# Kernel optimization log

Hardware: AMD Instinct MI355X
Metric: run time of the kernel (lower is better)

The kernel has to match this reference:

```python
import jax, jax.numpy as jnp
import numpy as np

B, N, G, E = 4, 8192, 512, 512
D = 3 * E  # fused channel dim = 1536
BN_EPS = 1e-5


def setup_inputs() -> dict:
    key = jax.random.key(0)
    ks = jax.random.split(key, 8)
    f32 = jnp.float32
    return {
        "xyz": jax.random.normal(ks[0], (B, N, 3), f32),
        "centers": jax.random.normal(ks[1], (B, G, 3), f32),
        "H4": jax.random.normal(ks[2], (B, G, E), f32),
        "H8": jax.random.normal(ks[3], (B, G, E), f32),
        "H12": jax.random.normal(ks[4], (B, G, E), f32),
        "w1": jax.random.normal(ks[5], (512, D), f32) * 0.02,
        "b1": jnp.zeros((512,), f32),
        "g1": jnp.ones((512,), f32),
        "be1": jnp.zeros((512,), f32),
        "m1": jnp.zeros((512,), f32),
        "v1": jnp.ones((512,), f32),
        "w2": jax.random.normal(ks[6], (512, 512), f32) * 0.02,
        "b2": jnp.zeros((512,), f32),
        "g2": jnp.ones((512,), f32),
        "be2": jnp.zeros((512,), f32),
        "m2": jnp.zeros((512,), f32),
        "v2": jnp.ones((512,), f32),
    }


def _bn(x, gamma, beta, mean, var):
    # BatchNorm1d, eval mode with running stats (per-channel, last axis)
    return (x - mean) * jax.lax.rsqrt(var + BN_EPS) * gamma + beta


def reference(xyz, centers, H4, H8, H12,
              w1, b1, g1, be1, m1, v1,
              w2, b2, g2, be2, m2, v2):
    fused = jnp.concatenate([H4, H8, H12], axis=-1)  # [B,G,D]
    # squared pairwise distances [B,N,G]
    d = (jnp.sum(xyz * xyz, axis=-1, keepdims=True)
         + jnp.sum(centers * centers, axis=-1)[:, None, :]
         - 2.0 * jnp.einsum('bnc,bgc->bng', xyz, centers))
    neg_d3, idx = jax.lax.top_k(-d, 3)  # 3 smallest distances, ascending
    d3 = -neg_d3  # [B,N,3]
    recip = 1.0 / (d3 + 1e-8)
    w = recip / jnp.sum(recip, axis=-1, keepdims=True)  # [B,N,3]
    # gather neighbor features: [B,N,3,D]
    gathered = jax.vmap(lambda f, i: f[i])(fused, idx)
    interp = jnp.einsum('bnk,bnkd->bnd', w, gathered)  # [B,N,D]
    # 1x1 conv == per-point linear; conv -> BN(eval) -> ReLU, twice
    h = jax.nn.relu(_bn(interp @ w1.T + b1, g1, be1, m1, v1))
    h = jax.nn.relu(_bn(h @ w2.T + b2, g2, be2, m2, v2))
    return h  # [B,N,512]
```

## Files before the change

### kernel.cpp

```cpp
#include <hip/hip_runtime.h>
#include <stdint.h>

#define NB 4
#define NP 8192
#define NG 512
#define DF 1536
#define NC 512

using f32x4   = __attribute__((ext_vector_type(4))) float;
using bf16x8  = __attribute__((ext_vector_type(8))) __bf16;
using ushort8v = __attribute__((ext_vector_type(8))) unsigned short;


__device__ __forceinline__ unsigned short f32_to_bf16(float f) {
  unsigned int u = __float_as_uint(f);
  u += 0x7fffu + ((u >> 16) & 1u);
  return (unsigned short)(u >> 16);
}

__global__ __launch_bounds__(256) void setup_kernel(
    const float* __restrict__ xyz, const float* __restrict__ centers,
    const float* __restrict__ H4, const float* __restrict__ H8,
    const float* __restrict__ H12,
    const float* __restrict__ w1, const float* __restrict__ w2,
    const float* __restrict__ g1, const float* __restrict__ be1,
    const float* __restrict__ m1, const float* __restrict__ v1,
    const float* __restrict__ g2, const float* __restrict__ be2,
    const float* __restrict__ m2, const float* __restrict__ v2,
    unsigned short* __restrict__ fswz, unsigned short* __restrict__ w1s,
    unsigned short* __restrict__ w2s,
    int* __restrict__ oidx, float* __restrict__ ow,
    float* __restrict__ s1, float* __restrict__ t1,
    float* __restrict__ s2, float* __restrict__ t2)
{
  __shared__ float4 cs[4 * 129];
  const int bx = blockIdx.x, tid = threadIdx.x;

  if (bx < 512) {
    const int b = bx >> 7;
    for (int i = tid; i < NG; i += 256) {
      float c0 = centers[((size_t)b * NG + i) * 3 + 0];
      float c1 = centers[((size_t)b * NG + i) * 3 + 1];
      float c2 = centers[((size_t)b * NG + i) * 3 + 2];
      float4 v; v.x = c0; v.y = c1; v.z = c2; v.w = c0 * c0 + c1 * c1 + c2 * c2;
      cs[(i >> 7) * 129 + (i & 127)] = v;
    }
    __syncthreads();
    const int t = (bx & 127) * 256 + tid;
    const int p = t >> 2, q = t & 3;
    const size_t pi = (size_t)b * NP + p;
    const float x0 = xyz[pi * 3 + 0], x1 = xyz[pi * 3 + 1], x2 = xyz[pi * 3 + 2];
    const float xx = x0 * x0 + x1 * x1 + x2 * x2;
    float d0 = 3.4e38f, d1 = 3.4e38f, d2 = 3.4e38f;
    int i0 = 0, i1 = 0, i2 = 0;
    const int gbase = q * 128;
    const float4* csq = cs + q * 129;
#pragma unroll 4
    for (int j = 0; j < 128; ++j) {
      float4 c = csq[j];
      float d = xx + c.w - 2.0f * (x0 * c.x + x1 * c.y + x2 * c.z);
      int g = gbase + j;
      bool c0 = d < d0, c1 = d < d1, c2 = d < d2;
      float nd2 = c1 ? d1 : (c2 ? d : d2); int ni2 = c1 ? i1 : (c2 ? g : i2);
      float nd1 = c0 ? d0 : (c1 ? d : d1); int ni1 = c0 ? i0 : (c1 ? g : i1);
      d0 = c0 ? d : d0;                    i0 = c0 ? g : i0;
      d1 = nd1; i1 = ni1; d2 = nd2; i2 = ni2;
    }
#pragma unroll
    for (int off = 1; off <= 2; off <<= 1) {
      float e0 = __shfl_xor(d0, off), e1 = __shfl_xor(d1, off), e2 = __shfl_xor(d2, off);
      int j0 = __shfl_xor(i0, off), j1 = __shfl_xor(i1, off), j2 = __shfl_xor(i2, off);
#pragma unroll
      for (int s = 0; s < 3; ++s) {
        float e = (s == 0) ? e0 : (s == 1 ? e1 : e2);
        int   j = (s == 0) ? j0 : (s == 1 ? j1 : j2);
        bool c0 = (e < d0) || (e == d0 && j < i0);
        bool c1 = (e < d1) || (e == d1 && j < i1);
        bool c2 = (e < d2) || (e == d2 && j < i2);
        float nd2 = c1 ? d1 : (c2 ? e : d2); int ni2 = c1 ? i1 : (c2 ? j : i2);
        float nd1 = c0 ? d0 : (c1 ? e : d1); int ni1 = c0 ? i0 : (c1 ? j : i1);
        d0 = c0 ? e : d0;                    i0 = c0 ? j : i0;
        d1 = nd1; i1 = ni1; d2 = nd2; i2 = ni2;
      }
    }
    if (q == 0) {
      float r0 = 1.0f / (d0 + 1e-8f), r1 = 1.0f / (d1 + 1e-8f), r2 = 1.0f / (d2 + 1e-8f);
      float inv = 1.0f / (r0 + r1 + r2);
      ow[pi * 3 + 0] = r0 * inv; ow[pi * 3 + 1] = r1 * inv; ow[pi * 3 + 2] = r2 * inv;
      oidx[pi * 3 + 0] = i0; oidx[pi * 3 + 1] = i1; oidx[pi * 3 + 2] = i2;
    }
  } else if (bx < 2048) {
    const int qd = (bx - 512) * 256 + tid;
    const int L = qd & 63, t2 = qd >> 6;
    const int kc = t2 % 48, mg = t2 / 48;
    const int m = mg * 16 + (L & 15);
    const int k = kc * 32 + (L >> 4) * 8;
    const float* src = (k < 512) ? H4 : (k < 1024 ? H8 : H12);
    const float* sp = &src[(size_t)m * 512 + (k & 511)];
    float4 va = *(const float4*)sp, vb = *(const float4*)(sp + 4);
    ushort8v o;
    o[0] = f32_to_bf16(va.x); o[1] = f32_to_bf16(va.y);
    o[2] = f32_to_bf16(va.z); o[3] = f32_to_bf16(va.w);
    o[4] = f32_to_bf16(vb.x); o[5] = f32_to_bf16(vb.y);
    o[6] = f32_to_bf16(vb.z); o[7] = f32_to_bf16(vb.w);
    *(ushort8v*)&fswz[((size_t)(mg * 48 + kc)) * 512 + L * 8] = o;
  } else if (bx < 2432) {
    const int qd = (bx - 2048) * 256 + tid;
    const int L = qd & 63, t2 = qd >> 6;
    const int kc = t2 % 48, ng = t2 / 48;
    const int n = ng * 16 + (L & 15);
    const int k = kc * 32 + (L >> 4) * 8;
    const float* sp = &w1[(size_t)n * 1536 + k];
    float4 va = *(const float4*)sp, vb = *(const float4*)(sp + 4);
    ushort8v o;
    o[0] = f32_to_bf16(va.x); o[1] = f32_to_bf16(va.y);
    o[2] = f32_to_bf16(va.z); o[3] = f32_to_bf16(va.w);
    o[4] = f32_to_bf16(vb.x); o[5] = f32_to_bf16(vb.y);
    o[6] = f32_to_bf16(vb.z); o[7] = f32_to_bf16(vb.w);
    *(ushort8v*)&w1s[((size_t)(ng * 48 + kc)) * 512 + L * 8] = o;
  } else if (bx < 2560) {
    const int qd = (bx - 2432) * 256 + tid;
    const int L = qd & 63, t2 = qd >> 6;
    const int kc = t2 & 15, ng = t2 >> 4;
    const int n = ng * 16 + (L & 15);
    const int k = kc * 32 + (L >> 4) * 8;
    const float* sp = &w2[(size_t)n * 512 + k];
    float4 va = *(const float4*)sp, vb = *(const float4*)(sp + 4);
    ushort8v o;
    o[0] = f32_to_bf16(va.x); o[1] = f32_to_bf16(va.y);
    o[2] = f32_to_bf16(va.z); o[3] = f32_to_bf16(va.w);
    o[4] = f32_to_bf16(vb.x); o[5] = f32_to_bf16(vb.y);
    o[6] = f32_to_bf16(vb.z); o[7] = f32_to_bf16(vb.w);
    *(ushort8v*)&w2s[((size_t)(ng * 16 + kc)) * 512 + L * 8] = o;
  } else {
    for (int i = tid; i < 512; i += 256) {
      float sa = g1[i] / sqrtf(v1[i] + 1e-5f);
      s1[i] = sa; t1[i] = be1[i] - m1[i] * sa;
      float sb = g2[i] / sqrtf(v2[i] + 1e-5f);
      s2[i] = sb; t2[i] = be2[i] - m2[i] * sb;
    }
  }
}

__global__ __launch_bounds__(256) void gemm1_kernel(
    const unsigned short* __restrict__ Aswz, const unsigned short* __restrict__ Bswz,
    float* __restrict__ Amat,
    const float* __restrict__ svec, const float* __restrict__ bvec,
    const float* __restrict__ tvec)
{
  __shared__ float red[64 * 65];
  const int tid = threadIdx.x, lane = tid & 63, wv = tid >> 6;
  const int m0 = (blockIdx.x >> 3) * 64;
  const int n0 = (blockIdx.x & 7) * 64;

  const unsigned short* Ap = Aswz + ((size_t)((m0 >> 4)) * 48 + wv * 12) * 512 + lane * 8;
  const unsigned short* Bp = Bswz + ((size_t)((n0 >> 4)) * 48 + wv * 12) * 512 + lane * 8;

  f32x4 acc[4][4];
#pragma unroll
  for (int i = 0; i < 4; ++i)
#pragma unroll
    for (int j = 0; j < 4; ++j) acc[i][j] = (f32x4){0.f, 0.f, 0.f, 0.f};

  bf16x8 af[4], bfr[4], afn[4], bfn[4];
#pragma unroll
  for (int i = 0; i < 4; ++i) {
    af[i]  = __builtin_bit_cast(bf16x8, *(const ushort8v*)(Ap + (size_t)i * 48 * 512));
    bfr[i] = __builtin_bit_cast(bf16x8, *(const ushort8v*)(Bp + (size_t)i * 48 * 512));
  }
#pragma unroll 1
  for (int kc = 0; kc < 12; ++kc) {
    if (kc < 11) {
#pragma unroll
      for (int i = 0; i < 4; ++i) {
        afn[i] = __builtin_bit_cast(bf16x8, *(const ushort8v*)(Ap + (size_t)i * 48 * 512 + (kc + 1) * 512));
        bfn[i] = __builtin_bit_cast(bf16x8, *(const ushort8v*)(Bp + (size_t)i * 48 * 512 + (kc + 1) * 512));
      }
    }
#pragma unroll
    for (int mi = 0; mi < 4; ++mi)
#pragma unroll
      for (int ni = 0; ni < 4; ++ni)
        acc[mi][ni] = __builtin_amdgcn_mfma_f32_16x16x32_bf16(af[mi], bfr[ni], acc[mi][ni], 0, 0, 0);
#pragma unroll
    for (int i = 0; i < 4; ++i) { af[i] = afn[i]; bfr[i] = bfn[i]; }
  }

  for (int w = 0; w < 4; ++w) {
    if (wv == w) {
#pragma unroll
      for (int mi = 0; mi < 4; ++mi)
#pragma unroll
        for (int ni = 0; ni < 4; ++ni) {
          int col = ni * 16 + (lane & 15);
#pragma unroll
          for (int r = 0; r < 4; ++r) {
            int row = mi * 16 + (lane >> 4) * 4 + r;
            if (w == 0) red[row * 65 + col] = acc[mi][ni][r];
            else        red[row * 65 + col] += acc[mi][ni][r];
          }
        }
    }
    __syncthreads();
  }
#pragma unroll
  for (int i = 0; i < 4; ++i) {
    int row = (tid >> 4) + i * 16;
    int col = (tid & 15) * 4;
    float4 v = *(const float4*)&red[row * 65 + col];
    int n = n0 + col;
    v.x = svec[n + 0] * (v.x + bvec[n + 0]) + tvec[n + 0];
    v.y = svec[n + 1] * (v.y + bvec[n + 1]) + tvec[n + 1];
    v.z = svec[n + 2] * (v.z + bvec[n + 2]) + tvec[n + 2];
    v.w = svec[n + 3] * (v.w + bvec[n + 3]) + tvec[n + 3];
    *(float4*)&Amat[(size_t)(m0 + row) * 512 + n] = v;
  }
}

__global__ __launch_bounds__(256) void interp_kernel(
    const float* __restrict__ Amat, const int* __restrict__ nidx,
    const float* __restrict__ nw, unsigned short* __restrict__ h1s)
{
  const int lane = threadIdx.x & 63, wv = threadIdx.x >> 6;
  const int pg = blockIdx.x * 4 + wv;
  const int p = pg * 16 + (lane & 15);
  const int b = p >> 13;
  const int i0 = nidx[p * 3 + 0], i1 = nidx[p * 3 + 1], i2 = nidx[p * 3 + 2];
  const float w0 = nw[p * 3 + 0], w1v = nw[p * 3 + 1], w2v = nw[p * 3 + 2];
  const float* A0 = Amat + ((size_t)(b * 512 + i0)) * 512;
  const float* A1 = Amat + ((size_t)(b * 512 + i1)) * 512;
  const float* A2 = Amat + ((size_t)(b * 512 + i2)) * 512;
  const int cbase = (lane >> 4) * 8;
  unsigned short* wp = h1s + ((size_t)pg * 16) * 512 + lane * 8;
#pragma unroll 4
  for (int cc = 0; cc < 16; ++cc) {
    const int c = cc * 32 + cbase;
    float4 a0a = *(const float4*)&A0[c], a0b = *(const float4*)&A0[c + 4];
    float4 a1a = *(const float4*)&A1[c], a1b = *(const float4*)&A1[c + 4];
    float4 a2a = *(const float4*)&A2[c], a2b = *(const float4*)&A2[c + 4];
    ushort8v o;
    o[0] = f32_to_bf16(fmaxf(w0 * a0a.x + w1v * a1a.x + w2v * a2a.x, 0.f));
    o[1] = f32_to_bf16(fmaxf(w0 * a0a.y + w1v * a1a.y + w2v * a2a.y, 0.f));
    o[2] = f32_to_bf16(fmaxf(w0 * a0a.z + w1v * a1a.z + w2v * a2a.z, 0.f));
    o[3] = f32_to_bf16(fmaxf(w0 * a0a.w + w1v * a1a.w + w2v * a2a.w, 0.f));
    o[4] = f32_to_bf16(fmaxf(w0 * a0b.x + w1v * a1b.x + w2v * a2b.x, 0.f));
    o[5] = f32_to_bf16(fmaxf(w0 * a0b.y + w1v * a1b.y + w2v * a2b.y, 0.f));
    o[6] = f32_to_bf16(fmaxf(w0 * a0b.z + w1v * a1b.z + w2v * a2b.z, 0.f));
    o[7] = f32_to_bf16(fmaxf(w0 * a0b.w + w1v * a1b.w + w2v * a2b.w, 0.f));
    *(ushort8v*)(wp + (size_t)cc * 512) = o;
  }
}

__global__ __launch_bounds__(256) void gemm2_kernel(
    const unsigned short* __restrict__ Aswz, const unsigned short* __restrict__ Bswz,
    float* __restrict__ outp,
    const float* __restrict__ svec, const float* __restrict__ bvec,
    const float* __restrict__ tvec)
{
  const int tid = threadIdx.x, lane = tid & 63, wv = tid >> 6;
  const int wm = wv >> 1, wn = wv & 1;
  const int L = blockIdx.x;
  const int xcd = L & 7, slot = L >> 3;
  const int mloc = slot >> 2, nt = slot & 3;
  const int m0 = (xcd * 32 + mloc) * 128, n0 = nt * 128;

  const unsigned short* Ap = Aswz + ((size_t)((m0 >> 4) + wm * 4) * 16) * 512 + lane * 8;
  const unsigned short* Bp = Bswz + ((size_t)((n0 >> 4) + wn * 4) * 16) * 512 + lane * 8;

  f32x4 acc[4][4];
#pragma unroll
  for (int i = 0; i < 4; ++i)
#pragma unroll
    for (int j = 0; j < 4; ++j) acc[i][j] = (f32x4){0.f, 0.f, 0.f, 0.f};

  bf16x8 af[4], bfr[4], afn[4], bfn[4];
#pragma unroll
  for (int i = 0; i < 4; ++i) {
    af[i]  = __builtin_bit_cast(bf16x8, *(const ushort8v*)(Ap + (size_t)i * 16 * 512));
    bfr[i] = __builtin_bit_cast(bf16x8, *(const ushort8v*)(Bp + (size_t)i * 16 * 512));
  }
#pragma unroll 1
  for (int kc = 0; kc < 16; ++kc) {
    if (kc < 15) {
#pragma unroll
      for (int i = 0; i < 4; ++i) {
        afn[i] = __builtin_bit_cast(bf16x8, *(const ushort8v*)(Ap + (size_t)i * 16 * 512 + (kc + 1) * 512));
        bfn[i] = __builtin_bit_cast(bf16x8, *(const ushort8v*)(Bp + (size_t)i * 16 * 512 + (kc + 1) * 512));
      }
    }
#pragma unroll
    for (int mi = 0; mi < 4; ++mi)
#pragma unroll
      for (int ni = 0; ni < 4; ++ni)
        acc[mi][ni] = __builtin_amdgcn_mfma_f32_16x16x32_bf16(af[mi], bfr[ni], acc[mi][ni], 0, 0, 0);
#pragma unroll
    for (int i = 0; i < 4; ++i) { af[i] = afn[i]; bfr[i] = bfn[i]; }
  }

#pragma unroll
  for (int mi = 0; mi < 4; ++mi) {
    int mbase = m0 + wm * 64 + mi * 16 + (lane >> 4) * 4;
#pragma unroll
    for (int ni = 0; ni < 4; ++ni) {
      int n = n0 + wn * 64 + ni * 16 + (lane & 15);
      float s = svec[n], bb = bvec[n], t = tvec[n];
      f32x4 v = acc[mi][ni];
#pragma unroll
      for (int r = 0; r < 4; ++r) {
        float val = fmaxf(s * (v[r] + bb) + t, 0.f);
        outp[(size_t)(mbase + r) * 512 + n] = val;
      }
    }
  }
}

extern "C" void kernel_launch(void* const* d_in, const int* in_sizes, int n_in,
                              void* d_out, int out_size, void* d_ws, size_t ws_size,
                              hipStream_t stream) {
  const float* xyz     = (const float*)d_in[0];
  const float* centers = (const float*)d_in[1];
  const float* H4      = (const float*)d_in[2];
  const float* H8      = (const float*)d_in[3];
  const float* H12     = (const float*)d_in[4];
  const float* w1      = (const float*)d_in[5];
  const float* b1      = (const float*)d_in[6];
  const float* g1      = (const float*)d_in[7];
  const float* be1     = (const float*)d_in[8];
  const float* m1      = (const float*)d_in[9];
  const float* v1      = (const float*)d_in[10];
  const float* w2      = (const float*)d_in[11];
  const float* b2      = (const float*)d_in[12];
  const float* g2      = (const float*)d_in[13];
  const float* be2     = (const float*)d_in[14];
  const float* m2      = (const float*)d_in[15];
  const float* v2      = (const float*)d_in[16];
  float* outp = (float*)d_out;

  char* ws = (char*)d_ws;
  unsigned short* fswz = (unsigned short*)(ws);
  unsigned short* w1s  = (unsigned short*)(ws + 6291456);
  unsigned short* w2s  = (unsigned short*)(ws + 7864320);
  float*          Amat = (float*)         (ws + 8388608);
  unsigned short* h1s  = (unsigned short*)(ws + 12582912);
  int*            nidx = (int*)           (ws + 46137344);
  float*          nw   = (float*)         (ws + 46530560);
  float*          s1   = (float*)         (ws + 46923776);
  float* t1 = s1 + 512; float* s2 = t1 + 512; float* t2 = s2 + 512;

  setup_kernel<<<2561, 256, 0, stream>>>(
      xyz, centers, H4, H8, H12, w1, w2,
      g1, be1, m1, v1, g2, be2, m2, v2,
      fswz, w1s, w2s, nidx, nw, s1, t1, s2, t2);
  gemm1_kernel<<<256, 256, 0, stream>>>(fswz, w1s, Amat, s1, b1, t1);
  interp_kernel<<<512, 256, 0, stream>>>(Amat, nidx, nw, h1s);
  gemm2_kernel<<<1024, 256, 0, stream>>>(h1s, w2s, outp, s2, b2, t2);
}
```

Baseline: 188.4 us.

## Fuse all stages into one cooperative persistent kernel with grid syncs and bf16 intermediate

Merges setup, gemm1, interpolation and gemm2 into a single cooperative kernel of 512 blocks that loops over work units and separates phases with grid-wide syncs, removing the gaps between kernel launches. The gemm1 output is now stored as bf16 instead of fp32, which halves the traffic for the gather-heavy interpolation. gemm1 tiles shrink to 32 rows so its work spreads over 512 blocks. A fallback path launches the four phases as separate kernels if cooperative launch fails. The costs are grid-sync overhead, a launch-bound occupancy limit, and an extra bf16 rounding before interpolation.

```diff
diff --git a/kernel.cpp b/kernel.cpp
--- a/kernel.cpp
+++ b/kernel.cpp
@@ -1,14 +1,15 @@
 #include <hip/hip_runtime.h>
+#include <hip/hip_cooperative_groups.h>
 #include <stdint.h>
 
-#define NB 4
 #define NP 8192
 #define NG 512
 #define DF 1536
-#define NC 512
-
-using f32x4   = __attribute__((ext_vector_type(4))) float;
-using bf16x8  = __attribute__((ext_vector_type(8))) __bf16;
+
+namespace cg = cooperative_groups;
+
+using f32x4    = __attribute__((ext_vector_type(4))) float;
+using bf16x8   = __attribute__((ext_vector_type(8))) __bf16;
 using ushort8v = __attribute__((ext_vector_type(8))) unsigned short;
 
 
@@ -17,39 +18,35 @@
   u += 0x7fffu + ((u >> 16) & 1u);
   return (unsigned short)(u >> 16);
 }
-
-__global__ __launch_bounds__(256) void setup_kernel(
-    const float* __restrict__ xyz, const float* __restrict__ centers,
-    const float* __restrict__ H4, const float* __restrict__ H8,
-    const float* __restrict__ H12,
-    const float* __restrict__ w1, const float* __restrict__ w2,
-    const float* __restrict__ g1, const float* __restrict__ be1,
-    const float* __restrict__ m1, const float* __restrict__ v1,
-    const float* __restrict__ g2, const float* __restrict__ be2,
-    const float* __restrict__ m2, const float* __restrict__ v2,
-    unsigned short* __restrict__ fswz, unsigned short* __restrict__ w1s,
-    unsigned short* __restrict__ w2s,
-    int* __restrict__ oidx, float* __restrict__ ow,
-    float* __restrict__ s1, float* __restrict__ t1,
-    float* __restrict__ s2, float* __restrict__ t2)
-{
-  __shared__ float4 cs[4 * 129];
-  const int bx = blockIdx.x, tid = threadIdx.x;
-
-  if (bx < 512) {
-    const int b = bx >> 7;
+__device__ __forceinline__ float bf2f(unsigned short u) {
+  return __uint_as_float(((unsigned)u) << 16);
+}
+
+struct FusedArgs {
+  const float *xyz, *centers, *H4, *H8, *H12, *w1, *w2;
+  const float *g1, *be1, *m1, *v1, *g2, *be2, *m2, *v2, *b1, *b2;
+  unsigned short *fswz, *w1s, *w2s, *Amatb, *h1s;
+  int *nidx; float *nw, *s1, *t1, *s2, *t2;
+  float *outp;
+};
+
+__device__ void phase_setup(const FusedArgs& a, char* smem, int w) {
+  const int tid = threadIdx.x;
+  if (w < 512) {
+    float4* cs = (float4*)smem;
+    const int b = w >> 7;
     for (int i = tid; i < NG; i += 256) {
-      float c0 = centers[((size_t)b * NG + i) * 3 + 0];
-      float c1 = centers[((size_t)b * NG + i) * 3 + 1];
-      float c2 = centers[((size_t)b * NG + i) * 3 + 2];
+      float c0 = a.centers[((size_t)b * NG + i) * 3 + 0];
+      float c1 = a.centers[((size_t)b * NG + i) * 3 + 1];
+      float c2 = a.centers[((size_t)b * NG + i) * 3 + 2];
       float4 v; v.x = c0; v.y = c1; v.z = c2; v.w = c0 * c0 + c1 * c1 + c2 * c2;
       cs[(i >> 7) * 129 + (i & 127)] = v;
     }
     __syncthreads();
-    const int t = (bx & 127) * 256 + tid;
+    const int t = (w & 127) * 256 + tid;
     const int p = t >> 2, q = t & 3;
     const size_t pi = (size_t)b * NP + p;
-    const float x0 = xyz[pi * 3 + 0], x1 = xyz[pi * 3 + 1], x2 = xyz[pi * 3 + 2];
+    const float x0 = a.xyz[pi * 3 + 0], x1 = a.xyz[pi * 3 + 1], x2 = a.xyz[pi * 3 + 2];
     const float xx = x0 * x0 + x1 * x1 + x2 * x2;
     float d0 = 3.4e38f, d1 = 3.4e38f, d2 = 3.4e38f;
     int i0 = 0, i1 = 0, i2 = 0;
@@ -86,16 +83,17 @@
     if (q == 0) {
       float r0 = 1.0f / (d0 + 1e-8f), r1 = 1.0f / (d1 + 1e-8f), r2 = 1.0f / (d2 + 1e-8f);
       float inv = 1.0f / (r0 + r1 + r2);
-      ow[pi * 3 + 0] = r0 * inv; ow[pi * 3 + 1] = r1 * inv; ow[pi * 3 + 2] = r2 * inv;
-      oidx[pi * 3 + 0] = i0; oidx[pi * 3 + 1] = i1; oidx[pi * 3 + 2] = i2;
-    }
-  } else if (bx < 2048) {
-    const int qd = (bx - 512) * 256 + tid;
+      a.nw[pi * 3 + 0] = r0 * inv; a.nw[pi * 3 + 1] = r1 * inv; a.nw[pi * 3 + 2] = r2 * inv;
+      a.nidx[pi * 3 + 0] = i0; a.nidx[pi * 3 + 1] = i1; a.nidx[pi * 3 + 2] = i2;
+    }
+    __syncthreads();
+  } else if (w < 2048) {
+    const int qd = (w - 512) * 256 + tid;
     const int L = qd & 63, t2 = qd >> 6;
     const int kc = t2 % 48, mg = t2 / 48;
     const int m = mg * 16 + (L & 15);
     const int k = kc * 32 + (L >> 4) * 8;
-    const float* src = (k < 512) ? H4 : (k < 1024 ? H8 : H12);
+    const float* src = (k < 512) ? a.H4 : (k < 1024 ? a.H8 : a.H12);
     const float* sp = &src[(size_t)m * 512 + (k & 511)];
     float4 va = *(const float4*)sp, vb = *(const float4*)(sp + 4);
     ushort8v o;
@@ -103,93 +101,92 @@
     o[2] = f32_to_bf16(va.z); o[3] = f32_to_bf16(va.w);
     o[4] = f32_to_bf16(vb.x); o[5] = f32_to_bf16(vb.y);
     o[6] = f32_to_bf16(vb.z); o[7] = f32_to_bf16(vb.w);
-    *(ushort8v*)&fswz[((size_t)(mg * 48 + kc)) * 512 + L * 8] = o;
-  } else if (bx < 2432) {
-    const int qd = (bx - 2048) * 256 + tid;
+    *(ushort8v*)&a.fswz[((size_t)(mg * 48 + kc)) * 512 + L * 8] = o;
+  } else if (w < 2432) {
+    const int qd = (w - 2048) * 256 + tid;
     const int L = qd & 63, t2 = qd >> 6;
     const int kc = t2 % 48, ng = t2 / 48;
     const int n = ng * 16 + (L & 15);
     const int k = kc * 32 + (L >> 4) * 8;
-    const float* sp = &w1[(size_t)n * 1536 + k];
+    const float* sp = &a.w1[(size_t)n * 1536 + k];
     float4 va = *(const float4*)sp, vb = *(const float4*)(sp + 4);
     ushort8v o;
     o[0] = f32_to_bf16(va.x); o[1] = f32_to_bf16(va.y);
     o[2] = f32_to_bf16(va.z); o[3] = f32_to_bf16(va.w);
     o[4] = f32_to_bf16(vb.x); o[5] = f32_to_bf16(vb.y);
     o[6] = f32_to_bf16(vb.z); o[7] = f32_to_bf16(vb.w);
-    *(ushort8v*)&w1s[((size_t)(ng * 48 + kc)) * 512 + L * 8] = o;
-  } else if (bx < 2560) {
-    const int qd = (bx - 2432) * 256 + tid;
+    *(ushort8v*)&a.w1s[((size_t)(ng * 48 + kc)) * 512 + L * 8] = o;
+  } else if (w < 2560) {
+    const int qd = (w - 2432) * 256 + tid;
     const int L = qd & 63, t2 = qd >> 6;
     const int kc = t2 & 15, ng = t2 >> 4;
     const int n = ng * 16 + (L & 15);
     const int k = kc * 32 + (L >> 4) * 8;
-    const float* sp = &w2[(size_t)n * 512 + k];
+    const float* sp = &a.w2[(size_t)n * 512 + k];
     float4 va = *(const float4*)sp, vb = *(const float4*)(sp + 4);
     ushort8v o;
     o[0] = f32_to_bf16(va.x); o[1] = f32_to_bf16(va.y);
     o[2] = f32_to_bf16(va.z); o[3] = f32_to_bf16(va.w);
     o[4] = f32_to_bf16(vb.x); o[5] = f32_to_bf16(vb.y);
     o[6] = f32_to_bf16(vb.z); o[7] = f32_to_bf16(vb.w);
-    *(ushort8v*)&w2s[((size_t)(ng * 16 + kc)) * 512 + L * 8] = o;
+    *(ushort8v*)&a.w2s[((size_t)(ng * 16 + kc)) * 512 + L * 8] = o;
   } else {
     for (int i = tid; i < 512; i += 256) {
-      float sa = g1[i] / sqrtf(v1[i] + 1e-5f);
-      s1[i] = sa; t1[i] = be1[i] - m1[i] * sa;
-      float sb = g2[i] / sqrtf(v2[i] + 1e-5f);
-      s2[i] = sb; t2[i] = be2[i] - m2[i] * sb;
-    }
-  }
-}
-
-__global__ __launch_bounds__(256) void gemm1_kernel(
-    const unsigned short* __restrict__ Aswz, const unsigned short* __restrict__ Bswz,
-    float* __restrict__ Amat,
-    const float* __restrict__ svec, const float* __restrict__ bvec,
-    const float* __restrict__ tvec)
-{
-  __shared__ float red[64 * 65];
+      float sa = a.g1[i] / sqrtf(a.v1[i] + 1e-5f);
+      a.s1[i] = sa; a.t1[i] = a.be1[i] - a.m1[i] * sa;
+      float sb = a.g2[i] / sqrtf(a.v2[i] + 1e-5f);
+      a.s2[i] = sb; a.t2[i] = a.be2[i] - a.m2[i] * sb;
+    }
+  }
+}
+
+__device__ void phase_gemm1(const FusedArgs& a, char* smem) {
+  float* red = (float*)smem;
   const int tid = threadIdx.x, lane = tid & 63, wv = tid >> 6;
-  const int m0 = (blockIdx.x >> 3) * 64;
-  const int n0 = (blockIdx.x & 7) * 64;
-
-  const unsigned short* Ap = Aswz + ((size_t)((m0 >> 4)) * 48 + wv * 12) * 512 + lane * 8;
-  const unsigned short* Bp = Bswz + ((size_t)((n0 >> 4)) * 48 + wv * 12) * 512 + lane * 8;
-
-  f32x4 acc[4][4];
+  const int blk = blockIdx.x;
+  const int m0 = (blk >> 3) * 32;
+  const int n0 = (blk & 7) * 64;
+  const unsigned short* Ap = a.fswz + ((size_t)(m0 >> 4) * 48 + wv * 12) * 512 + lane * 8;
+  const unsigned short* Bp = a.w1s  + ((size_t)(n0 >> 4) * 48 + wv * 12) * 512 + lane * 8;
+
+  f32x4 acc[2][4];
+#pragma unroll
+  for (int i = 0; i < 2; ++i)
+#pragma unroll
+    for (int j = 0; j < 4; ++j) acc[i][j] = (f32x4){0.f, 0.f, 0.f, 0.f};
+
+  bf16x8 af[2], bfr[4], afn[2], bfn[4];
+#pragma unroll
+  for (int i = 0; i < 2; ++i)
+    af[i]  = __builtin_bit_cast(bf16x8, *(const ushort8v*)(Ap + (size_t)i * 48 * 512));
 #pragma unroll
   for (int i = 0; i < 4; ++i)
-#pragma unroll
-    for (int j = 0; j < 4; ++j) acc[i][j] = (f32x4){0.f, 0.f, 0.f, 0.f};
-
-  bf16x8 af[4], bfr[4], afn[4], bfn[4];
-#pragma unroll
-  for (int i = 0; i < 4; ++i) {
-    af[i]  = __builtin_bit_cast(bf16x8, *(const ushort8v*)(Ap + (size_t)i * 48 * 512));
     bfr[i] = __builtin_bit_cast(bf16x8, *(const ushort8v*)(Bp + (size_t)i * 48 * 512));
-  }
 #pragma unroll 1
   for (int kc = 0; kc < 12; ++kc) {
     if (kc < 11) {
 #pragma unroll
-      for (int i = 0; i < 4; ++i) {
+      for (int i = 0; i < 2; ++i)
         afn[i] = __builtin_bit_cast(bf16x8, *(const ushort8v*)(Ap + (size_t)i * 48 * 512 + (kc + 1) * 512));
+#pragma unroll
+      for (int i = 0; i < 4; ++i)
         bfn[i] = __builtin_bit_cast(bf16x8, *(const ushort8v*)(Bp + (size_t)i * 48 * 512 + (kc + 1) * 512));
-      }
-    }
-#pragma unroll
-    for (int mi = 0; mi < 4; ++mi)
+    }
+#pragma unroll
+    for (int mi = 0; mi < 2; ++mi)
 #pragma unroll
       for (int ni = 0; ni < 4; ++ni)
         acc[mi][ni] = __builtin_amdgcn_mfma_f32_16x16x32_bf16(af[mi], bfr[ni], acc[mi][ni], 0, 0, 0);
 #pragma unroll
-    for (int i = 0; i < 4; ++i) { af[i] = afn[i]; bfr[i] = bfn[i]; }
+    for (int i = 0; i < 2; ++i) af[i] = afn[i];
+#pragma unroll
+    for (int i = 0; i < 4; ++i) bfr[i] = bfn[i];
   }
 
   for (int w = 0; w < 4; ++w) {
     if (wv == w) {
 #pragma unroll
-      for (int mi = 0; mi < 4; ++mi)
+      for (int mi = 0; mi < 2; ++mi)
 #pragma unroll
         for (int ni = 0; ni < 4; ++ni) {
           int col = ni * 16 + (lane & 15);
@@ -203,69 +200,55 @@
     }
     __syncthreads();
   }
-#pragma unroll
-  for (int i = 0; i < 4; ++i) {
-    int row = (tid >> 4) + i * 16;
-    int col = (tid & 15) * 4;
-    float4 v = *(const float4*)&red[row * 65 + col];
-    int n = n0 + col;
-    v.x = svec[n + 0] * (v.x + bvec[n + 0]) + tvec[n + 0];
-    v.y = svec[n + 1] * (v.y + bvec[n + 1]) + tvec[n + 1];
-    v.z = svec[n + 2] * (v.z + bvec[n + 2]) + tvec[n + 2];
-    v.w = svec[n + 3] * (v.w + bvec[n + 3]) + tvec[n + 3];
-    *(float4*)&Amat[(size_t)(m0 + row) * 512 + n] = v;
-  }
-}
-
-__global__ __launch_bounds__(256) void interp_kernel(
-    const float* __restrict__ Amat, const int* __restrict__ nidx,
-    const float* __restrict__ nw, unsigned short* __restrict__ h1s)
-{
-  const int lane = threadIdx.x & 63, wv = threadIdx.x >> 6;
+  const int row = tid >> 3;
+  const int col = (tid & 7) * 8;
+  ushort8v o;
+#pragma unroll
+  for (int j = 0; j < 8; ++j) {
+    int n = n0 + col + j;
+    float v = red[row * 65 + col + j];
+    o[j] = f32_to_bf16(a.s1[n] * (v + a.b1[n]) + a.t1[n]);
+  }
+  *(ushort8v*)&a.Amatb[(size_t)(m0 + row) * 512 + n0 + col] = o;
+}
+
+__device__ void phase_interp(const FusedArgs& a) {
+  const int tid = threadIdx.x, lane = tid & 63, wv = tid >> 6;
   const int pg = blockIdx.x * 4 + wv;
   const int p = pg * 16 + (lane & 15);
   const int b = p >> 13;
-  const int i0 = nidx[p * 3 + 0], i1 = nidx[p * 3 + 1], i2 = nidx[p * 3 + 2];
-  const float w0 = nw[p * 3 + 0], w1v = nw[p * 3 + 1], w2v = nw[p * 3 + 2];
-  const float* A0 = Amat + ((size_t)(b * 512 + i0)) * 512;
-  const float* A1 = Amat + ((size_t)(b * 512 + i1)) * 512;
-  const float* A2 = Amat + ((size_t)(b * 512 + i2)) * 512;
+  const int i0 = a.nidx[p * 3 + 0], i1 = a.nidx[p * 3 + 1], i2 = a.nidx[p * 3 + 2];
+  const float w0 = a.nw[p * 3 + 0], w1v = a.nw[p * 3 + 1], w2v = a.nw[p * 3 + 2];
+  const unsigned short* A0 = a.Amatb + ((size_t)(b * 512 + i0)) * 512;
+  const unsigned short* A1 = a.Amatb + ((size_t)(b * 512 + i1)) * 512;
+  const unsigned short* A2 = a.Amatb + ((size_t)(b * 512 + i2)) * 512;
   const int cbase = (lane >> 4) * 8;
-  unsigned short* wp = h1s + ((size_t)pg * 16) * 512 + lane * 8;
+  unsigned short* wp = a.h1s + ((size_t)pg * 16) * 512 + lane * 8;
 #pragma unroll 4
   for (int cc = 0; cc < 16; ++cc) {
     const int c = cc * 32 + cbase;
-    float4 a0a = *(const float4*)&A0[c], a0b = *(const float4*)&A0[c + 4];
-    float4 a1a = *(const float4*)&A1[c], a1b = *(const float4*)&A1[c + 4];
-    float4 a2a = *(const float4*)&A2[c], a2b = *(const float4*)&A2[c + 4];
+    ushort8v u0 = *(const ushort8v*)&A0[c];
+    ushort8v u1 = *(const ushort8v*)&A1[c];
+    ushort8v u2 = *(const ushort8v*)&A2[c];
     ushort8v o;
-    o[0] = f32_to_bf16(fmaxf(w0 * a0a.x + w1v * a1a.x + w2v * a2a.x, 0.f));
-    o[1] = f32_to_bf16(fmaxf(w0 * a0a.y + w1v * a1a.y + w2v * a2a.y, 0.f));
-    o[2] = f32_to_bf16(fmaxf(w0 * a0a.z + w1v * a1a.z + w2v * a2a.z, 0.f));
-    o[3] = f32_to_bf16(fmaxf(w0 * a0a.w + w1v * a1a.w + w2v * a2a.w, 0.f));
-    o[4] = f32_to_bf16(fmaxf(w0 * a0b.x + w1v * a1b.x + w2v * a2b.x, 0.f));
-    o[5] = f32_to_bf16(fmaxf(w0 * a0b.y + w1v * a1b.y + w2v * a2b.y, 0.f));
-    o[6] = f32_to_bf16(fmaxf(w0 * a0b.z + w1v * a1b.z + w2v * a2b.z, 0.f));
-    o[7] = f32_to_bf16(fmaxf(w0 * a0b.w + w1v * a1b.w + w2v * a2b.w, 0.f));
+#pragma unroll
+    for (int j = 0; j < 8; ++j) {
+      float v = w0 * bf2f(u0[j]) + w1v * bf2f(u1[j]) + w2v * bf2f(u2[j]);
+      o[j] = f32_to_bf16(fmaxf(v, 0.f));
+    }
     *(ushort8v*)(wp + (size_t)cc * 512) = o;
   }
 }
 
-__global__ __launch_bounds__(256) void gemm2_kernel(
-    const unsigned short* __restrict__ Aswz, const unsigned short* __restrict__ Bswz,
-    float* __restrict__ outp,
-    const float* __restrict__ svec, const float* __restrict__ bvec,
-    const float* __restrict__ tvec)
-{
+__device__ void phase_gemm2(const FusedArgs& a, int L) {
   const int tid = threadIdx.x, lane = tid & 63, wv = tid >> 6;
   const int wm = wv >> 1, wn = wv & 1;
-  const int L = blockIdx.x;
   const int xcd = L & 7, slot = L >> 3;
   const int mloc = slot >> 2, nt = slot & 3;
   const int m0 = (xcd * 32 + mloc) * 128, n0 = nt * 128;
 
-  const unsigned short* Ap = Aswz + ((size_t)((m0 >> 4) + wm * 4) * 16) * 512 + lane * 8;
-  const unsigned short* Bp = Bswz + ((size_t)((n0 >> 4) + wn * 4) * 16) * 512 + lane * 8;
+  const unsigned short* Ap = a.h1s + ((size_t)((m0 >> 4) + wm * 4) * 16) * 512 + lane * 8;
+  const unsigned short* Bp = a.w2s + ((size_t)((n0 >> 4) + wn * 4) * 16) * 512 + lane * 8;
 
   f32x4 acc[4][4];
 #pragma unroll
@@ -303,55 +286,92 @@
 #pragma unroll
     for (int ni = 0; ni < 4; ++ni) {
       int n = n0 + wn * 64 + ni * 16 + (lane & 15);
-      float s = svec[n], bb = bvec[n], t = tvec[n];
+      float s = a.s2[n], bb = a.b2[n], t = a.t2[n];
       f32x4 v = acc[mi][ni];
 #pragma unroll
       for (int r = 0; r < 4; ++r) {
         float val = fmaxf(s * (v[r] + bb) + t, 0.f);
-        outp[(size_t)(mbase + r) * 512 + n] = val;
+        a.outp[(size_t)(mbase + r) * 512 + n] = val;
       }
     }
   }
+}
+
+__global__ __launch_bounds__(256, 2) void fused_kernel(FusedArgs a) {
+  __shared__ __align__(16) char smem[8448];
+  cg::grid_group grid = cg::this_grid();
+  const int blk = blockIdx.x;
+  for (int u = blk; u <= 2560; u += 512) phase_setup(a, smem, u);
+  grid.sync();
+  phase_gemm1(a, smem);
+  grid.sync();
+  phase_interp(a);
+  grid.sync();
+  phase_gemm2(a, blk);
+  phase_gemm2(a, blk + 512);
+}
+
+__global__ __launch_bounds__(256) void k_setup(FusedArgs a) {
+  __shared__ __align__(16) char smem[8448];
+  for (int u = blockIdx.x; u <= 2560; u += 512) phase_setup(a, smem, u);
+}
+__global__ __launch_bounds__(256) void k_gemm1(FusedArgs a) {
+  __shared__ __align__(16) char smem[8448];
+  phase_gemm1(a, smem);
+}
+__global__ __launch_bounds__(256) void k_interp(FusedArgs a) { phase_interp(a); }
+__global__ __launch_bounds__(256) void k_gemm2(FusedArgs a) {
+  phase_gemm2(a, blockIdx.x);
+  phase_gemm2(a, blockIdx.x + 512);
 }
 
 extern "C" void kernel_launch(void* const* d_in, const int* in_sizes, int n_in,
                               void* d_out, int out_size, void* d_ws, size_t ws_size,
                               hipStream_t stream) {
-  const float* xyz     = (const float*)d_in[0];
-  const float* centers = (const float*)d_in[1];
-  const float* H4      = (const float*)d_in[2];
-  const float* H8      = (const float*)d_in[3];
-  const float* H12     = (const float*)d_in[4];
-  const float* w1      = (const float*)d_in[5];
-  const float* b1      = (const float*)d_in[6];
-  const float* g1      = (const float*)d_in[7];
-  const float* be1     = (const float*)d_in[8];
-  const float* m1      = (const float*)d_in[9];
-  const float* v1      = (const float*)d_in[10];
-  const float* w2      = (const float*)d_in[11];
-  const float* b2      = (const float*)d_in[12];
-  const float* g2      = (const float*)d_in[13];
-  const float* be2     = (const float*)d_in[14];
-  const float* m2      = (const float*)d_in[15];
-  const float* v2      = (const float*)d_in[16];
-  float* outp = (float*)d_out;
-
   char* ws = (char*)d_ws;
-  unsigned short* fswz = (unsigned short*)(ws);
-  unsigned short* w1s  = (unsigned short*)(ws + 6291456);
-  unsigned short* w2s  = (unsigned short*)(ws + 7864320);
-  float*          Amat = (float*)         (ws + 8388608);
-  unsigned short* h1s  = (unsigned short*)(ws + 12582912);
-  int*            nidx = (int*)           (ws + 46137344);
-  float*          nw   = (float*)         (ws + 46530560);
-  float*          s1   = (float*)         (ws + 46923776);
-  float* t1 = s1 + 512; float* s2 = t1 + 512; float* t2 = s2 + 512;
-
-  setup_kernel<<<2561, 256, 0, stream>>>(
-      xyz, centers, H4, H8, H12, w1, w2,
-      g1, be1, m1, v1, g2, be2, m2, v2,
-      fswz, w1s, w2s, nidx, nw, s1, t1, s2, t2);
-  gemm1_kernel<<<256, 256, 0, stream>>>(fswz, w1s, Amat, s1, b1, t1);
-  interp_kernel<<<512, 256, 0, stream>>>(Amat, nidx, nw, h1s);
-  gemm2_kernel<<<1024, 256, 0, stream>>>(h1s, w2s, outp, s2, b2, t2);
-}
+  FusedArgs a;
+  a.xyz     = (const float*)d_in[0];
+  a.centers = (const float*)d_in[1];
+  a.H4      = (const float*)d_in[2];
+  a.H8      = (const float*)d_in[3];
+  a.H12     = (const float*)d_in[4];
+  a.w1      = (const float*)d_in[5];
+  a.b1      = (const float*)d_in[6];
+  a.g1      = (const float*)d_in[7];
+  a.be1     = (const float*)d_in[8];
+  a.m1      = (const float*)d_in[9];
+  a.v1      = (const float*)d_in[10];
+  a.w2      = (const float*)d_in[11];
+  a.b2      = (const float*)d_in[12];
+  a.g2      = (const float*)d_in[13];
+  a.be2     = (const float*)d_in[14];
+  a.m2      = (const float*)d_in[15];
+  a.v2      = (const float*)d_in[16];
+  a.fswz  = (unsigned short*)(ws);
+  a.w1s   = (unsigned short*)(ws + 6291456);
+  a.w2s   = (unsigned short*)(ws + 7864320);
+  a.Amatb = (unsigned short*)(ws + 8388608);
+  a.h1s   = (unsigned short*)(ws + 12582912);
+  a.nidx  = (int*)           (ws + 46137344);
+  a.nw    = (float*)         (ws + 46530560);
+  a.s1    = (float*)         (ws + 46923776);
+  a.t1 = a.s1 + 512; a.s2 = a.t1 + 512; a.t2 = a.s2 + 512;
+  a.outp  = (float*)d_out;
+
+  int nb = 0;
+  hipError_t qerr = hipOccupancyMaxActiveBlocksPerMultiprocessor(
+      &nb, reinterpret_cast<const void*>(fused_kernel), 256, 0);
+  bool coop_ok = (qerr == hipSuccess) && (nb >= 2);
+  if (coop_ok) {
+    void* kp[] = { (void*)&a };
+    hipError_t lerr = hipLaunchCooperativeKernel(
+        (const void*)fused_kernel, dim3(512), dim3(256), kp, 0, stream);
+    coop_ok = (lerr == hipSuccess);
+  }
+  if (!coop_ok) {
+    k_setup <<<512, 256, 0, stream>>>(a);
+    k_gemm1 <<<512, 256, 0, stream>>>(a);
+    k_interp<<<512, 256, 0, stream>>>(a);
+    k_gemm2 <<<512, 256, 0, stream>>>(a);
+  }
+}
```

Result: faster. 178.0 us (-5.5%).
